# Kernel optimization log

Hardware: AMD Instinct MI355X
Metric: run time of the kernel (lower is better)

The kernel has to match this reference:

```python
import jax, jax.numpy as jnp
import numpy as np

N, E, F_IN, HID, EPS = 50000, 800000, 128, 256, 1e-5

def _glorot(key, shape):
    scale = 1.0 / np.sqrt(shape[0])
    return jax.random.uniform(key, shape, jnp.float32, -scale, scale)

def setup_inputs() -> dict:
    key = jax.random.key(0)
    ks = jax.random.split(key, 20)
    x = jax.random.normal(ks[0], (N, F_IN), jnp.float32)
    edge_index = jax.random.randint(ks[1], (2, E), 0, N, jnp.int64)
    inp = {"x": x, "edge_index": edge_index}
    dims = [F_IN, HID, HID]
    for i in range(3):
        d_in = dims[i]
        inp[f"Wn{i}"] = _glorot(ks[2 + 4 * i], (d_in, HID))      # lin_l weight (neighbors), with bias
        inp[f"bn{i}"] = jnp.zeros((HID,), jnp.float32)
        inp[f"Wr{i}"] = _glorot(ks[3 + 4 * i], (d_in, HID))      # lin_r weight (root), no bias
        inp[f"g{i}"] = jnp.ones((HID,), jnp.float32)              # BN gamma
        inp[f"b{i}"] = jnp.zeros((HID,), jnp.float32)             # BN beta
    return inp

def _sage_bn_elu(x, src, dst, Wn, bn, Wr, g, b):
    # mean aggregation of source features onto destination nodes
    agg = jax.ops.segment_sum(x[src], dst, num_segments=N)                      # [N, d_in]
    deg = jax.ops.segment_sum(jnp.ones((src.shape[0],), x.dtype), dst, num_segments=N)
    agg = agg / jnp.maximum(deg, 1.0)[:, None]
    h = agg @ Wn + bn + x @ Wr                                                  # SAGEConv(root_weight=True)
    mu = jnp.mean(h, axis=0)
    var = jnp.mean((h - mu) ** 2, axis=0)                                       # biased var (BN training)
    h = (h - mu) * jax.lax.rsqrt(var + EPS) * g + b
    return jnp.where(h > 0, h, jnp.expm1(h))                                    # ELU(alpha=1)

def reference(x, edge_index, Wn0, bn0, Wr0, g0, b0, Wn1, bn1, Wr1, g1, b1, Wn2, bn2, Wr2, g2, b2):
    src, dst = edge_index[0], edge_index[1]
    h = _sage_bn_elu(x, src, dst, Wn0, bn0, Wr0, g0, b0)
    h = _sage_bn_elu(h, src, dst, Wn1, bn1, Wr1, g1, b1)
    h = _sage_bn_elu(h, src, dst, Wn2, bn2, Wr2, g2, b2)
    return h
```

## Files before the change

### kernel.cpp

```cpp
#include <hip/hip_runtime.h>
#include <math.h>

#define N_NODES 50000
#define N_EDGES 800000
#define F_IN    128
#define HID     256
#define BN_EPS  1e-5f
#define SCAN_BLOCKS ((N_NODES + 255) / 256)

typedef unsigned int uint;
typedef __attribute__((ext_vector_type(8))) short bf16x8;
typedef __attribute__((ext_vector_type(4))) float f32x4;

__device__ __forceinline__ float bf2f(unsigned short u) {
    return __uint_as_float((uint)u << 16);
}
__device__ __forceinline__ unsigned short f2bf(float f) {
    uint u = __float_as_uint(f);
    return (unsigned short)((u + 0x7FFFu + ((u >> 16) & 1u)) >> 16);
}

__device__ __forceinline__ void gload16(const unsigned short* g, unsigned short* l) {
    __builtin_amdgcn_global_load_lds(
        (const __attribute__((address_space(1))) void*)g,
        (__attribute__((address_space(3))) void*)l, 16, 0, 0);
}

__global__ void hist_kernel(const int* __restrict__ dst, int* __restrict__ deg) {
    int e = blockIdx.x * blockDim.x + threadIdx.x;
    if (e < N_EDGES) atomicAdd(&deg[dst[e]], 1);
}

__global__ __launch_bounds__(256) void scan1_kernel(const int* __restrict__ deg,
                                                    int* __restrict__ row_ptr,
                                                    int* __restrict__ partials) {
    __shared__ int sm[256];
    int i = blockIdx.x * 256 + threadIdx.x;
    int v = (i < N_NODES) ? deg[i] : 0;
    sm[threadIdx.x] = v;
    __syncthreads();
    for (int off = 1; off < 256; off <<= 1) {
        int t = (threadIdx.x >= off) ? sm[threadIdx.x - off] : 0;
        __syncthreads();
        sm[threadIdx.x] += t;
        __syncthreads();
    }
    if (i < N_NODES) row_ptr[i] = sm[threadIdx.x] - v;
    if (threadIdx.x == 255) partials[blockIdx.x] = sm[255];
}

__global__ __launch_bounds__(256) void scan2_kernel(int* __restrict__ partials) {
    __shared__ int sm[256];
    int t = threadIdx.x;
    int v = (t < SCAN_BLOCKS) ? partials[t] : 0;
    sm[t] = v;
    __syncthreads();
    for (int off = 1; off < 256; off <<= 1) {
        int p = (t >= off) ? sm[t - off] : 0;
        __syncthreads();
        sm[t] += p;
        __syncthreads();
    }
    if (t < SCAN_BLOCKS) partials[t] = sm[t] - v;
}

__global__ __launch_bounds__(256) void scan3_kernel(int* __restrict__ row_ptr,
                                                    int* __restrict__ cursor,
                                                    const int* __restrict__ partials) {
    int i = blockIdx.x * 256 + threadIdx.x;
    if (i < N_NODES) {
        int v = row_ptr[i] + partials[blockIdx.x];
        row_ptr[i] = v;
        cursor[i]  = v;
    }
    if (i == 0) row_ptr[N_NODES] = N_EDGES;
}

__global__ void fill_kernel(const int* __restrict__ src, const int* __restrict__ dst,
                            int* __restrict__ cursor, int* __restrict__ csr_src) {
    int e = blockIdx.x * blockDim.x + threadIdx.x;
    if (e >= N_EDGES) return;
    int pos = atomicAdd(&cursor[dst[e]], 1);
    csr_src[pos] = src[e];
}

__global__ void cast_bf16_kernel(const float* __restrict__ x, unsigned short* __restrict__ xb,
                                 int total4) {
    int i = blockIdx.x * blockDim.x + threadIdx.x;
    if (i >= total4) return;
    float4 v = *(const float4*)&x[(long)i * 4];
    unsigned short o[4] = {f2bf(v.x), f2bf(v.y), f2bf(v.z), f2bf(v.w)};
    *(uint2*)&xb[(long)i * 4] = *(const uint2*)o;
}

__global__ __launch_bounds__(256) void wt_kernel(const float* __restrict__ Wn,
                                                 const float* __restrict__ Wr,
                                                 int K1, int KT, unsigned short* __restrict__ WT) {
    int n  = threadIdx.x;
    int k0 = blockIdx.x * 16;
    unsigned short o[16];
#pragma unroll
    for (int j = 0; j < 16; ++j) {
        int k = k0 + j;
        float v = (k < K1) ? Wn[k * HID + n] : Wr[(k - K1) * HID + n];
        o[j] = f2bf(v);
    }
    *(uint4*)&WT[(long)n * KT + k0]     = *(const uint4*)&o[0];
    *(uint4*)&WT[(long)n * KT + k0 + 8] = *(const uint4*)&o[8];
}

template<int D>
__global__ __launch_bounds__(256) void gather_mean_kernel(
    const unsigned short* __restrict__ x, const int* __restrict__ row_ptr,
    const int* __restrict__ csr_src, unsigned short* __restrict__ agg) {
    constexpr int VPL = D / 64;
    int node = blockIdx.x * 4 + (threadIdx.x >> 6);
    int lane = threadIdx.x & 63;
    if (node >= N_NODES) return;
    int beg = row_ptr[node], end = row_ptr[node + 1];
    float acc[VPL];
#pragma unroll
    for (int j = 0; j < VPL; j++) acc[j] = 0.f;
    int e = beg;
    for (; e + 4 <= end; e += 4) {
        int s0 = csr_src[e], s1 = csr_src[e + 1], s2 = csr_src[e + 2], s3 = csr_src[e + 3];
        if constexpr (VPL == 4) {
            uint2 v0 = *(const uint2*)&x[(long)s0 * D + lane * 4];
            uint2 v1 = *(const uint2*)&x[(long)s1 * D + lane * 4];
            uint2 v2 = *(const uint2*)&x[(long)s2 * D + lane * 4];
            uint2 v3 = *(const uint2*)&x[(long)s3 * D + lane * 4];
            acc[0] += (bf2f((unsigned short)(v0.x & 0xFFFF)) + bf2f((unsigned short)(v1.x & 0xFFFF)))
                    + (bf2f((unsigned short)(v2.x & 0xFFFF)) + bf2f((unsigned short)(v3.x & 0xFFFF)));
            acc[1] += (bf2f((unsigned short)(v0.x >> 16))    + bf2f((unsigned short)(v1.x >> 16)))
                    + (bf2f((unsigned short)(v2.x >> 16))    + bf2f((unsigned short)(v3.x >> 16)));
            acc[2] += (bf2f((unsigned short)(v0.y & 0xFFFF)) + bf2f((unsigned short)(v1.y & 0xFFFF)))
                    + (bf2f((unsigned short)(v2.y & 0xFFFF)) + bf2f((unsigned short)(v3.y & 0xFFFF)));
            acc[3] += (bf2f((unsigned short)(v0.y >> 16))    + bf2f((unsigned short)(v1.y >> 16)))
                    + (bf2f((unsigned short)(v2.y >> 16))    + bf2f((unsigned short)(v3.y >> 16)));
        } else {
            uint v0 = *(const uint*)&x[(long)s0 * D + lane * 2];
            uint v1 = *(const uint*)&x[(long)s1 * D + lane * 2];
            uint v2 = *(const uint*)&x[(long)s2 * D + lane * 2];
            uint v3 = *(const uint*)&x[(long)s3 * D + lane * 2];
            acc[0] += (bf2f((unsigned short)(v0 & 0xFFFF)) + bf2f((unsigned short)(v1 & 0xFFFF)))
                    + (bf2f((unsigned short)(v2 & 0xFFFF)) + bf2f((unsigned short)(v3 & 0xFFFF)));
            acc[1] += (bf2f((unsigned short)(v0 >> 16))    + bf2f((unsigned short)(v1 >> 16)))
                    + (bf2f((unsigned short)(v2 >> 16))    + bf2f((unsigned short)(v3 >> 16)));
        }
    }
    for (; e < end; e++) {
        int s0 = csr_src[e];
        if constexpr (VPL == 4) {
            uint2 v0 = *(const uint2*)&x[(long)s0 * D + lane * 4];
            acc[0] += bf2f((unsigned short)(v0.x & 0xFFFF));
            acc[1] += bf2f((unsigned short)(v0.x >> 16));
            acc[2] += bf2f((unsigned short)(v0.y & 0xFFFF));
            acc[3] += bf2f((unsigned short)(v0.y >> 16));
        } else {
            uint v0 = *(const uint*)&x[(long)s0 * D + lane * 2];
            acc[0] += bf2f((unsigned short)(v0 & 0xFFFF));
            acc[1] += bf2f((unsigned short)(v0 >> 16));
        }
    }
    float inv = 1.0f / fmaxf((float)(end - beg), 1.0f);
    unsigned short* o = &agg[(long)node * D + lane * VPL];
    if constexpr (VPL == 4) {
        unsigned short ov[4] = {f2bf(acc[0] * inv), f2bf(acc[1] * inv),
                                f2bf(acc[2] * inv), f2bf(acc[3] * inv)};
        *(uint2*)o = *(const uint2*)ov;
    } else {
        unsigned short ov[2] = {f2bf(acc[0] * inv), f2bf(acc[1] * inv)};
        *(uint*)o = *(const uint*)ov;
    }
}

template<int K1, int K2>
__global__ __launch_bounds__(256) void mfma_gemm_kernel(
    const unsigned short* __restrict__ A1, const unsigned short* __restrict__ A2,
    const unsigned short* __restrict__ WT, const float* __restrict__ bias,
    unsigned short* __restrict__ Hout, float* __restrict__ s12) {
    constexpr int KT = K1 + K2;
    constexpr int NITER = KT / 64;
    __shared__ unsigned short As[2][128 * 64];
    __shared__ unsigned short Bs[2][128 * 64];
    __shared__ float cs[128];
    __shared__ float cq[128];

    const int tid  = threadIdx.x;
    const int wave = tid >> 6;
    const int lane = tid & 63;
    const int m16  = lane & 15;
    const int quad = lane >> 4;
    const int row_block = blockIdx.x >> 1;
    const int col_half  = blockIdx.x & 1;
    const int r0 = row_block * 128;
    const int rl = lane >> 3;
    const int cl = lane & 7;
    const int csw = cl ^ rl;

    if (tid < 128) { cs[tid] = 0.f; cq[tid] = 0.f; }

    f32x4 acc[2][8];
#pragma unroll
    for (int mt = 0; mt < 2; mt++)
#pragma unroll
        for (int nt = 0; nt < 8; nt++) acc[mt][nt] = (f32x4){0.f, 0.f, 0.f, 0.f};

    auto stage = [&](int buf, int k0) {
        const unsigned short* Ab;
        int pitch, kk;
        if (k0 < K1) { Ab = A1; pitch = K1; kk = k0; }
        else         { Ab = A2; pitch = K2; kk = k0 - K1; }
#pragma unroll
        for (int j = 0; j < 4; ++j) {
            int lr = wave * 32 + j * 8 + rl;
            long gr = min(r0 + lr, N_NODES - 1);
            gload16(&Ab[gr * pitch + kk + csw * 8], &As[buf][(wave * 32 + j * 8) * 64]);
        }
#pragma unroll
        for (int j = 0; j < 4; ++j) {
            int lr = wave * 32 + j * 8 + rl;
            long gn = col_half * 128 + lr;
            gload16(&WT[gn * KT + k0 + csw * 8], &Bs[buf][(wave * 32 + j * 8) * 64]);
        }
    };

    stage(0, 0);
    asm volatile("s_waitcnt vmcnt(0)" ::: "memory");
    __builtin_amdgcn_s_barrier();

#pragma unroll
    for (int it = 0; it < NITER; ++it) {
        const int cur = it & 1;
        if (it + 1 < NITER) stage(cur ^ 1, (it + 1) * 64);
#pragma unroll
        for (int ks = 0; ks < 2; ++ks) {
            bf16x8 afrag[2], bfrag[8];
#pragma unroll
            for (int mt = 0; mt < 2; mt++) {
                int ar = wave * 32 + mt * 16 + m16;
                afrag[mt] = *(const bf16x8*)&As[cur][ar * 64 + (((ks * 4 + quad) ^ (m16 & 7)) * 8)];
            }
#pragma unroll
            for (int nt = 0; nt < 8; nt++) {
                int br = nt * 16 + m16;
                bfrag[nt] = *(const bf16x8*)&Bs[cur][br * 64 + (((ks * 4 + quad) ^ (m16 & 7)) * 8)];
            }
#pragma unroll
            for (int mt = 0; mt < 2; mt++)
#pragma unroll
                for (int nt = 0; nt < 8; nt++)
                    acc[mt][nt] = __builtin_amdgcn_mfma_f32_16x16x32_bf16(
                        afrag[mt], bfrag[nt], acc[mt][nt], 0, 0, 0);
        }
        asm volatile("s_waitcnt vmcnt(0)" ::: "memory");
        __builtin_amdgcn_s_barrier();
    }

#pragma unroll
    for (int nt = 0; nt < 8; nt++) {
        int lcol = nt * 16 + m16;
        int col  = col_half * 128 + lcol;
        float bv = bias[col];
        float s = 0.f, q = 0.f;
#pragma unroll
        for (int mt = 0; mt < 2; mt++) {
#pragma unroll
            for (int reg = 0; reg < 4; reg++) {
                int row = r0 + wave * 32 + mt * 16 + quad * 4 + reg;
                float v = acc[mt][nt][reg] + bv;
                if (row < N_NODES) {
                    Hout[(long)row * HID + col] = f2bf(v);
                    s += v;
                    q += v * v;
                }
            }
        }
        atomicAdd(&cs[lcol], s);
        atomicAdd(&cq[lcol], q);
    }
    __syncthreads();
    if (tid < 128) {
        atomicAdd(&s12[col_half * 128 + tid], cs[tid]);
        atomicAdd(&s12[HID + col_half * 128 + tid], cq[tid]);
    }
}

__global__ void bn_prep_kernel(const float* __restrict__ s12, const float* __restrict__ g,
                               const float* __restrict__ b, float* __restrict__ ss) {
    int c = threadIdx.x;
    float mu  = s12[c] * (1.0f / N_NODES);
    float var = s12[HID + c] * (1.0f / N_NODES) - mu * mu;
    var = fmaxf(var, 0.f);
    float sc = rsqrtf(var + BN_EPS) * g[c];
    ss[c]       = sc;
    ss[HID + c] = b[c] - mu * sc;
}

template<bool OUT32>
__global__ void bn_elu_kernel(const unsigned short* __restrict__ h, const float* __restrict__ ss,
                              void* __restrict__ out) {
    const int total4 = N_NODES * HID / 4;
    int i = blockIdx.x * blockDim.x + threadIdx.x;
    if (i >= total4) return;
    int c4 = (i % (HID / 4)) * 4;
    uint2 v = *(const uint2*)&h[(long)i * 4];
    float4 sc = *(const float4*)&ss[c4];
    float4 sh = *(const float4*)&ss[HID + c4];
    float in[4] = {bf2f((unsigned short)(v.x & 0xFFFF)), bf2f((unsigned short)(v.x >> 16)),
                   bf2f((unsigned short)(v.y & 0xFFFF)), bf2f((unsigned short)(v.y >> 16))};
    float scv[4] = {sc.x, sc.y, sc.z, sc.w};
    float shv[4] = {sh.x, sh.y, sh.z, sh.w};
    float o[4];
#pragma unroll
    for (int j = 0; j < 4; j++) {
        float t = fmaf(in[j], scv[j], shv[j]);
        o[j] = t > 0.f ? t : expm1f(t);
    }
    if (OUT32) {
        float4 ov = {o[0], o[1], o[2], o[3]};
        *(float4*)&((float*)out)[(long)i * 4] = ov;
    } else {
        unsigned short ov[4] = {f2bf(o[0]), f2bf(o[1]), f2bf(o[2]), f2bf(o[3])};
        *(uint2*)&((unsigned short*)out)[(long)i * 4] = *(const uint2*)ov;
    }
}

extern "C" void kernel_launch(void* const* d_in, const int* in_sizes, int n_in,
                              void* d_out, int out_size, void* d_ws, size_t ws_size,
                              hipStream_t stream) {
    const float* x   = (const float*)d_in[0];
    const int*   ei  = (const int*)d_in[1];
    const int*   src = ei;
    const int*   dst = ei + N_EDGES;
    const float* Wn[3] = {(const float*)d_in[2],  (const float*)d_in[7],  (const float*)d_in[12]};
    const float* bn[3] = {(const float*)d_in[3],  (const float*)d_in[8],  (const float*)d_in[13]};
    const float* Wr[3] = {(const float*)d_in[4],  (const float*)d_in[9],  (const float*)d_in[14]};
    const float* g [3] = {(const float*)d_in[5],  (const float*)d_in[10], (const float*)d_in[15]};
    const float* b [3] = {(const float*)d_in[6],  (const float*)d_in[11], (const float*)d_in[16]};
    float* out = (float*)d_out;

    const size_t BF = (size_t)N_NODES * HID * 2;
    char* ws = (char*)d_ws;
    unsigned short* B0  = (unsigned short*)(ws);
    unsigned short* B1  = (unsigned short*)(ws + BF);
    unsigned short* B2  = (unsigned short*)(ws + 2 * BF);
    unsigned short* XB  = (unsigned short*)(ws + 3 * BF);
    char* ws2 = ws + 3 * BF + (size_t)N_NODES * F_IN * 2;
    unsigned short* WT0 = (unsigned short*)(ws2);
    unsigned short* WT1 = (unsigned short*)(ws2 + 256 * 256 * 2);
    unsigned short* WT2 = (unsigned short*)(ws2 + 256 * 256 * 2 + 256 * 512 * 2);
    char* ws3 = ws2 + 256 * 256 * 2 + 2 * (256 * 512 * 2);
    int*   row_ptr = (int*)ws3;
    int*   cursor  = row_ptr + (N_NODES + 1);
    int*   deg_i   = cursor + N_NODES;
    int*   partial = deg_i + N_NODES;
    int*   csr_src = partial + SCAN_BLOCKS;
    float* s12     = (float*)(csr_src + N_EDGES);
    float* ss      = s12 + 3 * 2 * HID;

    const int eb = (N_EDGES + 255) / 256;
    const int gather_blocks = (N_NODES + 3) / 4;
    const int elu_blocks = (N_NODES * HID / 4 + 255) / 256;
    const int gemm_blocks = ((N_NODES + 127) / 128) * 2;

    hipMemsetAsync(deg_i, 0, N_NODES * sizeof(int), stream);
    hipMemsetAsync(s12, 0, 3 * 2 * HID * sizeof(float), stream);
    hist_kernel<<<eb, 256, 0, stream>>>(dst, deg_i);
    scan1_kernel<<<SCAN_BLOCKS, 256, 0, stream>>>(deg_i, row_ptr, partial);
    scan2_kernel<<<1, 256, 0, stream>>>(partial);
    scan3_kernel<<<SCAN_BLOCKS, 256, 0, stream>>>(row_ptr, cursor, partial);
    fill_kernel<<<eb, 256, 0, stream>>>(src, dst, cursor, csr_src);
    cast_bf16_kernel<<<(N_NODES * F_IN / 4 + 255) / 256, 256, 0, stream>>>(x, XB, N_NODES * F_IN / 4);
    wt_kernel<<<(2 * F_IN) / 16, 256, 0, stream>>>(Wn[0], Wr[0], F_IN, 2 * F_IN, WT0);
    wt_kernel<<<(2 * HID) / 16, 256, 0, stream>>>(Wn[1], Wr[1], HID, 2 * HID, WT1);
    wt_kernel<<<(2 * HID) / 16, 256, 0, stream>>>(Wn[2], Wr[2], HID, 2 * HID, WT2);

    gather_mean_kernel<F_IN><<<gather_blocks, 256, 0, stream>>>(XB, row_ptr, csr_src, B0);
    mfma_gemm_kernel<F_IN, F_IN><<<gemm_blocks, 256, 0, stream>>>(B0, XB, WT0, bn[0], B1, s12);
    bn_prep_kernel<<<1, 256, 0, stream>>>(s12, g[0], b[0], ss);
    bn_elu_kernel<false><<<elu_blocks, 256, 0, stream>>>(B1, ss, B2);

    gather_mean_kernel<HID><<<gather_blocks, 256, 0, stream>>>(B2, row_ptr, csr_src, B0);
    mfma_gemm_kernel<HID, HID><<<gemm_blocks, 256, 0, stream>>>(B0, B2, WT1, bn[1], B1, s12 + 2 * HID);
    bn_prep_kernel<<<1, 256, 0, stream>>>(s12 + 2 * HID, g[1], b[1], ss);
    bn_elu_kernel<false><<<elu_blocks, 256, 0, stream>>>(B1, ss, B2);

    gather_mean_kernel<HID><<<gather_blocks, 256, 0, stream>>>(B2, row_ptr, csr_src, B0);
    mfma_gemm_kernel<HID, HID><<<gemm_blocks, 256, 0, stream>>>(B0, B2, WT2, bn[2], B1, s12 + 4 * HID);
    bn_prep_kernel<<<1, 256, 0, stream>>>(s12 + 4 * HID, g[2], b[2], ss);
    bn_elu_kernel<true><<<elu_blocks, 256, 0, stream>>>(B1, ss, out);
}
```

Before: 560.2 us.

## Replace global BN atomics with per-block partials and tighten GEMM load pipelining

```diff
diff --git a/kernel.cpp b/kernel.cpp
--- a/kernel.cpp
+++ b/kernel.cpp
@@ -7,6 +7,7 @@
 #define HID     256
 #define BN_EPS  1e-5f
 #define SCAN_BLOCKS ((N_NODES + 255) / 256)
+#define ROW_BLOCKS  ((N_NODES + 127) / 128)
 
 typedef unsigned int uint;
 typedef __attribute__((ext_vector_type(8))) short bf16x8;
@@ -178,7 +179,7 @@
 __global__ __launch_bounds__(256) void mfma_gemm_kernel(
     const unsigned short* __restrict__ A1, const unsigned short* __restrict__ A2,
     const unsigned short* __restrict__ WT, const float* __restrict__ bias,
-    unsigned short* __restrict__ Hout, float* __restrict__ s12) {
+    unsigned short* __restrict__ Hout, float* __restrict__ sred) {
     constexpr int KT = K1 + K2;
     constexpr int NITER = KT / 64;
     __shared__ unsigned short As[2][128 * 64];
@@ -206,7 +207,9 @@
 #pragma unroll
         for (int nt = 0; nt < 8; nt++) acc[mt][nt] = (f32x4){0.f, 0.f, 0.f, 0.f};
 
-    auto stage = [&](int buf, int k0) {
+    auto issue = [&](int t) {
+        const int buf = t & 1;
+        const int k0  = t * 64;
         const unsigned short* Ab;
         int pitch, kk;
         if (k0 < K1) { Ab = A1; pitch = K1; kk = k0; }
@@ -225,14 +228,18 @@
         }
     };
 
-    stage(0, 0);
-    asm volatile("s_waitcnt vmcnt(0)" ::: "memory");
-    __builtin_amdgcn_s_barrier();
+    issue(0);
 
 #pragma unroll
     for (int it = 0; it < NITER; ++it) {
         const int cur = it & 1;
-        if (it + 1 < NITER) stage(cur ^ 1, (it + 1) * 64);
+        if (it + 1 < NITER) {
+            issue(it + 1);
+            asm volatile("s_waitcnt vmcnt(8)" ::: "memory");
+        } else {
+            asm volatile("s_waitcnt vmcnt(0)" ::: "memory");
+        }
+        __builtin_amdgcn_s_barrier();
 #pragma unroll
         for (int ks = 0; ks < 2; ++ks) {
             bf16x8 afrag[2], bfrag[8];
@@ -253,7 +260,6 @@
                     acc[mt][nt] = __builtin_amdgcn_mfma_f32_16x16x32_bf16(
                         afrag[mt], bfrag[nt], acc[mt][nt], 0, 0, 0);
         }
-        asm volatile("s_waitcnt vmcnt(0)" ::: "memory");
         __builtin_amdgcn_s_barrier();
     }
 
@@ -276,25 +282,50 @@
                 }
             }
         }
-        atomicAdd(&cs[lcol], s);
-        atomicAdd(&cq[lcol], q);
+        s += __shfl_xor(s, 16); s += __shfl_xor(s, 32);
+        q += __shfl_xor(q, 16); q += __shfl_xor(q, 32);
+        if (quad == 0) {
+            atomicAdd(&cs[lcol], s);
+            atomicAdd(&cq[lcol], q);
+        }
     }
     __syncthreads();
     if (tid < 128) {
-        atomicAdd(&s12[col_half * 128 + tid], cs[tid]);
-        atomicAdd(&s12[HID + col_half * 128 + tid], cq[tid]);
-    }
-}
-
-__global__ void bn_prep_kernel(const float* __restrict__ s12, const float* __restrict__ g,
-                               const float* __restrict__ b, float* __restrict__ ss) {
-    int c = threadIdx.x;
-    float mu  = s12[c] * (1.0f / N_NODES);
-    float var = s12[HID + c] * (1.0f / N_NODES) - mu * mu;
+        sred[(long)blockIdx.x * 256 + tid]       = cs[tid];
+        sred[(long)blockIdx.x * 256 + 128 + tid] = cq[tid];
+    }
+}
+
+__global__ __launch_bounds__(256) void bn_reduce_kernel(const float* __restrict__ sred,
+                                                        const float* __restrict__ g,
+                                                        const float* __restrict__ b,
+                                                        float* __restrict__ ss) {
+    int t  = threadIdx.x;
+    int hf = t >> 7;
+    int lc = t & 127;
+    float S[4] = {0.f, 0.f, 0.f, 0.f}, Q[4] = {0.f, 0.f, 0.f, 0.f};
+    int rb = 0;
+    for (; rb + 4 <= ROW_BLOCKS; rb += 4) {
+#pragma unroll
+        for (int u = 0; u < 4; u++) {
+            const float* p = &sred[(long)((rb + u) * 2 + hf) * 256 + lc];
+            S[u] += p[0];
+            Q[u] += p[128];
+        }
+    }
+    for (; rb < ROW_BLOCKS; rb++) {
+        const float* p = &sred[(long)(rb * 2 + hf) * 256 + lc];
+        S[0] += p[0];
+        Q[0] += p[128];
+    }
+    float Sv = (S[0] + S[1]) + (S[2] + S[3]);
+    float Qv = (Q[0] + Q[1]) + (Q[2] + Q[3]);
+    float mu  = Sv * (1.0f / N_NODES);
+    float var = Qv * (1.0f / N_NODES) - mu * mu;
     var = fmaxf(var, 0.f);
-    float sc = rsqrtf(var + BN_EPS) * g[c];
-    ss[c]       = sc;
-    ss[HID + c] = b[c] - mu * sc;
+    float sc = rsqrtf(var + BN_EPS) * g[t];
+    ss[t]       = sc;
+    ss[HID + t] = b[t] - mu * sc;
 }
 
 template<bool OUT32>
@@ -356,16 +387,15 @@
     int*   deg_i   = cursor + N_NODES;
     int*   partial = deg_i + N_NODES;
     int*   csr_src = partial + SCAN_BLOCKS;
-    float* s12     = (float*)(csr_src + N_EDGES);
-    float* ss      = s12 + 3 * 2 * HID;
+    float* sred    = (float*)(csr_src + N_EDGES);
+    float* ss      = sred + (size_t)ROW_BLOCKS * 2 * 256;
 
     const int eb = (N_EDGES + 255) / 256;
     const int gather_blocks = (N_NODES + 3) / 4;
     const int elu_blocks = (N_NODES * HID / 4 + 255) / 256;
-    const int gemm_blocks = ((N_NODES + 127) / 128) * 2;
+    const int gemm_blocks = ROW_BLOCKS * 2;
 
     hipMemsetAsync(deg_i, 0, N_NODES * sizeof(int), stream);
-    hipMemsetAsync(s12, 0, 3 * 2 * HID * sizeof(float), stream);
     hist_kernel<<<eb, 256, 0, stream>>>(dst, deg_i);
     scan1_kernel<<<SCAN_BLOCKS, 256, 0, stream>>>(deg_i, row_ptr, partial);
     scan2_kernel<<<1, 256, 0, stream>>>(partial);
@@ -377,17 +407,17 @@
     wt_kernel<<<(2 * HID) / 16, 256, 0, stream>>>(Wn[2], Wr[2], HID, 2 * HID, WT2);
 
     gather_mean_kernel<F_IN><<<gather_blocks, 256, 0, stream>>>(XB, row_ptr, csr_src, B0);
-    mfma_gemm_kernel<F_IN, F_IN><<<gemm_blocks, 256, 0, stream>>>(B0, XB, WT0, bn[0], B1, s12);
-    bn_prep_kernel<<<1, 256, 0, stream>>>(s12, g[0], b[0], ss);
+    mfma_gemm_kernel<F_IN, F_IN><<<gemm_blocks, 256, 0, stream>>>(B0, XB, WT0, bn[0], B1, sred);
+    bn_reduce_kernel<<<1, 256, 0, stream>>>(sred, g[0], b[0], ss);
     bn_elu_kernel<false><<<elu_blocks, 256, 0, stream>>>(B1, ss, B2);
 
     gather_mean_kernel<HID><<<gather_blocks, 256, 0, stream>>>(B2, row_ptr, csr_src, B0);
-    mfma_gemm_kernel<HID, HID><<<gemm_blocks, 256, 0, stream>>>(B0, B2, WT1, bn[1], B1, s12 + 2 * HID);
-    bn_prep_kernel<<<1, 256, 0, stream>>>(s12 + 2 * HID, g[1], b[1], ss);
+    mfma_gemm_kernel<HID, HID><<<gemm_blocks, 256, 0, stream>>>(B0, B2, WT1, bn[1], B1, sred);
+    bn_reduce_kernel<<<1, 256, 0, stream>>>(sred, g[1], b[1], ss);
     bn_elu_kernel<false><<<elu_blocks, 256, 0, stream>>>(B1, ss, B2);
 
     gather_mean_kernel<HID><<<gather_blocks, 256, 0, stream>>>(B2, row_ptr, csr_src, B0);
-    mfma_gemm_kernel<HID, HID><<<gemm_blocks, 256, 0, stream>>>(B0, B2, WT2, bn[2], B1, s12 + 4 * HID);
-    bn_prep_kernel<<<1, 256, 0, stream>>>(s12 + 4 * HID, g[2], b[2], ss);
+    mfma_gemm_kernel<HID, HID><<<gemm_blocks, 256, 0, stream>>>(B0, B2, WT2, bn[2], B1, sred);
+    bn_reduce_kernel<<<1, 256, 0, stream>>>(sred, g[2], b[2], ss);
     bn_elu_kernel<true><<<elu_blocks, 256, 0, stream>>>(B1, ss, out);
 }
```

After: 566.8 us. About the same (+1.2%).
